# Optimization experiments

Measured on AMD Instinct MI355X. Metric: run time of the kernel, lower is better.

## Reference

```python
import jax, jax.numpy as jnp
import numpy as np

BN_EPS = 1e-5
K2 = 9  # 3x3 kernel


def _conv3x3(x, w, b):
    # x: [B,C,H,W], w: [O,C,3,3] -> [B,O,H,W], stride 1, pad 1
    out = jax.lax.conv_general_dilated(
        x, w, window_strides=(1, 1), padding=((1, 1), (1, 1)),
        dimension_numbers=("NCHW", "OIHW", "NCHW"))
    return out + b[None, :, None, None]


def setup_inputs() -> dict:
    key = jax.random.key(0)
    ks = jax.random.split(key, 8)
    B, C, H, W = 8, 256, 64, 64
    O = 256
    x = jax.random.normal(ks[0], (B, C, H, W), dtype=jnp.float32)
    # offset/mask conv: small init so sampled offsets stay near the base grid
    w_off = jax.random.normal(ks[1], (3 * K2, C, 3, 3), dtype=jnp.float32) * 0.01
    b_off = jnp.zeros((3 * K2,), dtype=jnp.float32)
    weight = jax.random.normal(ks[2], (O, C, 3, 3), dtype=jnp.float32) * 0.02
    bias = jnp.zeros((O,), dtype=jnp.float32)
    gamma = jnp.ones((O,), dtype=jnp.float32)
    beta = jnp.zeros((O,), dtype=jnp.float32)
    run_mean = jax.random.normal(ks[3], (O,), dtype=jnp.float32) * 0.1
    run_var = jax.random.uniform(ks[4], (O,), dtype=jnp.float32) + 0.5
    return {"x": x, "w_off": w_off, "b_off": b_off, "weight": weight,
            "bias": bias, "gamma": gamma, "beta": beta,
            "run_mean": run_mean, "run_var": run_var}


def _deform_sample(img, py, px):
    # img: [C,H,W]; py, px: [K2,H,W] sampling coordinates.
    # Bilinear sample with zero padding outside (DCNv2 semantics:
    # out-of-bounds corners contribute zero).
    C, H, W = img.shape
    y0 = jnp.floor(py)
    x0 = jnp.floor(px)
    wy1 = py - y0  # frac weights for the 'high' corner
    wx1 = px - x0

    def gather(yi, xi):
        valid = (yi >= 0) & (yi < H) & (xi >= 0) & (xi < W)
        yc = jnp.clip(yi, 0, H - 1).astype(jnp.int32)
        xc = jnp.clip(xi, 0, W - 1).astype(jnp.int32)
        return img[:, yc, xc] * valid.astype(img.dtype)[None]  # [C,K2,H,W]

    v00 = gather(y0, x0)
    v01 = gather(y0, x0 + 1)
    v10 = gather(y0 + 1, x0)
    v11 = gather(y0 + 1, x0 + 1)
    return (v00 * ((1 - wy1) * (1 - wx1))[None]
            + v01 * ((1 - wy1) * wx1)[None]
            + v10 * (wy1 * (1 - wx1))[None]
            + v11 * (wy1 * wx1)[None])  # [C,K2,H,W]


def reference(x, w_off, b_off, weight, bias, gamma, beta, run_mean, run_var):
    B, C, H, W = x.shape
    O = weight.shape[0]
    # 1) offset / mask branch (standard 3x3 conv)
    om = _conv3x3(x, w_off, b_off)  # [B, 27, H, W]
    off_y = om[:, :K2]
    off_x = om[:, K2:2 * K2]
    mask = jax.nn.sigmoid(om[:, 2 * K2:])  # modulation, [B,9,H,W]
    # 2) base sampling grid for 3x3, stride 1, pad 1, dilation 1
    ky = jnp.repeat(jnp.arange(3), 3).astype(x.dtype)  # [9]
    kx = jnp.tile(jnp.arange(3), 3).astype(x.dtype)    # [9]
    hs = jnp.arange(H, dtype=x.dtype)
    ws = jnp.arange(W, dtype=x.dtype)
    base_y = hs[None, :, None] - 1.0 + ky[:, None, None]  # [9,H,1]
    base_x = ws[None, None, :] - 1.0 + kx[:, None, None]  # [9,1,W]
    py = base_y[None] + off_y  # [B,9,H,W]
    px = base_x[None] + off_x
    # 3) modulated deformable im2col (bilinear gather) per batch
    cols = jax.vmap(_deform_sample)(x, py, px)  # [B,C,9,H,W]
    cols = cols * mask[:, None]                 # apply modulation mask
    # 4) GEMM over (C, K2) + bias
    w3 = weight.reshape(O, C, K2)
    out = jnp.einsum("ock,bckhw->bohw", w3, cols) + bias[None, :, None, None]
    # 5) BatchNorm (eval mode, running stats) + ReLU
    inv = gamma / jnp.sqrt(run_var + BN_EPS)
    out = out * inv[None, :, None, None] + (beta - run_mean * inv)[None, :, None, None]
    return jax.nn.relu(out)
```

## Files before the change

kernel.cpp:

```cpp
#include <hip/hip_runtime.h>
#include <math.h>

#define H 64
#define W 64
#define C 256
#define O 256
#define CK 2304
#define NB 8
#define HWSZ 4096

typedef __attribute__((ext_vector_type(8))) short short8;
typedef __attribute__((ext_vector_type(4))) float floatx4;
typedef __attribute__((ext_vector_type(4))) unsigned uintx4;

#define FSWZ(n) ((((n) & 3) << 1) | (((n) >> 2) & 1))

__device__ __forceinline__ float lo2f(unsigned u) {
  return __builtin_bit_cast(float, u << 16);
}
__device__ __forceinline__ float hi2f(unsigned u) {
  return __builtin_bit_cast(float, u & 0xffff0000u);
}
__device__ __forceinline__ unsigned pk2bf(float v0, float v1) {
  unsigned a = __builtin_bit_cast(unsigned, v0);
  unsigned b = __builtin_bit_cast(unsigned, v1);
  return ((a + 0x8000u) >> 16) | ((b + 0x8000u) & 0xffff0000u);
}

__global__ __launch_bounds__(512) void prep_x(
    const float* __restrict__ x, unsigned short* __restrict__ xt) {
  __shared__ unsigned tile[16384];
  int bid = blockIdx.x;
  int tid = threadIdx.x;
  int b = bid >> 5;
  int yg = bid & 31;
  int y0 = yg * 2;

#pragma unroll
  for (int j = 0; j < 4; ++j) {
    int e = tid + 512 * j;
    int xx4 = e & 15;
    int cp = e >> 4;
    const float* p0 = x + ((size_t)b * C + 2 * cp) * HWSZ + y0 * W + xx4 * 4;
    floatx4 f00 = *reinterpret_cast<const floatx4*>(p0);
    floatx4 f01 = *reinterpret_cast<const floatx4*>(p0 + W);
    floatx4 f10 = *reinterpret_cast<const floatx4*>(p0 + HWSZ);
    floatx4 f11 = *reinterpret_cast<const floatx4*>(p0 + HWSZ + W);
    int sw = cp & 31;
#pragma unroll
    for (int k = 0; k < 4; ++k) {
      int px = xx4 * 4 + k;
      tile[cp * 64 + (px ^ sw)] = pk2bf(f00[k], f10[k]);
      tile[8192 + cp * 64 + (px ^ sw)] = pk2bf(f01[k], f11[k]);
    }
  }
  __syncthreads();

  unsigned short* xo = xt + ((size_t)(b * 64 + y0) << 14);
#pragma unroll
  for (int j = 0; j < 8; ++j) {
    int e = tid + 512 * j;
    int cq = e & 31;
    int xx = (e >> 5) & 63;
    int r = e >> 11;
    unsigned u[4];
#pragma unroll
    for (int kk = 0; kk < 4; ++kk) {
      int cpv = cq * 4 + kk;
      u[kk] = tile[r * 8192 + cpv * 64 + (xx ^ (cpv & 31))];
    }
    uint4 v = {u[0], u[1], u[2], u[3]};
    *reinterpret_cast<uint4*>(xo + (r << 14) + (xx << 8) + (cq << 3)) = v;
  }
}

__global__ __launch_bounds__(512) void prep_wb(
    const float* __restrict__ weight, const float* __restrict__ w_off,
    const float* __restrict__ bias, const float* __restrict__ gamma,
    const float* __restrict__ beta, const float* __restrict__ run_mean,
    const float* __restrict__ run_var, unsigned short* __restrict__ wb,
    unsigned short* __restrict__ wob, float* __restrict__ invsh) {
  int bid = blockIdx.x;
  int tid = threadIdx.x;

  if (bid < 144) {
    int idx = bid * 512 + tid;
    int d0 = idx * 8;
    int lane = idx & 63;
    int mt = (idx >> 6) & 15;
    int ks = idx >> 10;
    int o = mt * 16 + (lane & 15);
    int kn0 = ks * 32 + (lane >> 4) * 8;
    int tap = kn0 >> 8;
    int c0 = kn0 & 255;
    const float* wsrc = weight + o * CK + c0 * 9 + tap;
    unsigned pk[4];
#pragma unroll
    for (int p = 0; p < 4; ++p)
      pk[p] = pk2bf(wsrc[(2 * p) * 9], wsrc[(2 * p + 1) * 9]);
    uint4 v = {pk[0], pk[1], pk[2], pk[3]};
    *reinterpret_cast<uint4*>(wb + d0) = v;
  } else if (bid < 162) {
    int idx = (bid - 144) * 512 + tid;
    int d0 = idx * 8;
    int lane = idx & 63;
    int mt = (idx >> 6) & 1;
    int ks = idx >> 7;
    int o = mt * 16 + (lane & 15);
    int kn0 = ks * 32 + (lane >> 4) * 8;
    int tap = kn0 >> 8;
    int c0 = kn0 & 255;
    uint4 v;
    if (o < 27) {
      const float* wsrc = w_off + o * CK + c0 * 9 + tap;
      unsigned pk[4];
#pragma unroll
      for (int p = 0; p < 4; ++p)
        pk[p] = pk2bf(wsrc[(2 * p) * 9], wsrc[(2 * p + 1) * 9]);
      v = (uint4){pk[0], pk[1], pk[2], pk[3]};
    } else {
      v = (uint4){0, 0, 0, 0};
    }
    *reinterpret_cast<uint4*>(wob + d0) = v;
  } else {
    if (tid < 256) {
      int o = tid;
      float inv = gamma[o] * rsqrtf(run_var[o] + 1e-5f);
      invsh[o] = inv;
      invsh[O + o] = beta[o] + (bias[o] - run_mean[o]) * inv;
    }
  }
}

__global__ __launch_bounds__(512, 4) void deform_mfma_kernel(
    const unsigned short* __restrict__ xt, const unsigned short* __restrict__ wob,
    const float* __restrict__ b_off, const unsigned short* __restrict__ wb,
    const float* __restrict__ invsh, float* __restrict__ out) {
  __shared__ short cols[64 * 256];
  __shared__ float sm_om[27 * 64];
  __shared__ int sbase[576];
  __shared__ float s00[576], s01[576], s10[576], s11[576];

  int tid = threadIdx.x;
  int lane = tid & 63;
  int wvid = tid >> 6;
  int q = lane >> 4;
  int lm = lane & 15;
  int b = blockIdx.x;
  int h = blockIdx.y;
  const unsigned short* xtb = xt + ((size_t)b << 20);

  if (wvid < 4) {
    int mt = wvid & 1;
    int nh = wvid >> 1;
    floatx4 a0[2];
    a0[0] = (floatx4){0.f, 0.f, 0.f, 0.f};
    a0[1] = (floatx4){0.f, 0.f, 0.f, 0.f};
    int pxu[2];
    pxu[0] = (nh * 2 + 0) * 16 + lm;
    pxu[1] = (nh * 2 + 1) * 16 + lm;
    for (int tap = 0; tap < 9; ++tap) {
      int yy = h - 1 + tap / 3;
      bool vy = (yy >= 0) && (yy < H);
      const unsigned short* bp[2];
      bool vv[2];
#pragma unroll
      for (int u = 0; u < 2; ++u) {
        int xx = pxu[u] - 1 + tap % 3;
        vv[u] = vy && (xx >= 0) && (xx < W);
        bp[u] = xtb + ((((yy & 63) << 6) + (xx & 63)) << 8) + q * 8;
      }
#pragma unroll
      for (int s = 0; s < 8; ++s) {
        int ks = tap * 8 + s;
        short8 afrag = *reinterpret_cast<const short8*>(
            wob + (((ks * 2 + mt) * 64 + lane) << 3));
#pragma unroll
        for (int u = 0; u < 2; ++u) {
          short8 bfrag;
          if (vv[u])
            bfrag = *reinterpret_cast<const short8*>(bp[u] + s * 32);
          else
            bfrag = (short8){0, 0, 0, 0, 0, 0, 0, 0};
          a0[u] = __builtin_amdgcn_mfma_f32_16x16x32_bf16(afrag, bfrag, a0[u], 0, 0, 0);
        }
      }
    }
#pragma unroll
    for (int u = 0; u < 2; ++u)
#pragma unroll
      for (int r = 0; r < 4; ++r) {
        int o = mt * 16 + q * 4 + r;
        if (o < 27) sm_om[o * 64 + pxu[u]] = a0[u][r] + b_off[o];
      }
  }
  __syncthreads();

  for (int e = tid; e < 576; e += 512) {
    int n = e & 63;
    int k = e >> 6;
    float oy = sm_om[k * 64 + n];
    float ox = sm_om[(9 + k) * 64 + n];
    float mv = sm_om[(18 + k) * 64 + n];
    float m = 1.0f / (1.0f + __expf(-mv));
    float py = (float)(h - 1 + k / 3) + oy;
    float px = (float)(n - 1 + k % 3) + ox;
    float yf = floorf(py), xf = floorf(px);
    int y0 = (int)yf, x0 = (int)xf;
    float fy = py - yf, fx = px - xf;
    float r0, r1; int yl;
    if (y0 >= 0 && y0 <= H - 2)      { yl = y0;    r0 = 1.f - fy; r1 = fy;       }
    else if (y0 == -1)               { yl = 0;     r0 = fy;       r1 = 0.f;      }
    else if (y0 == H - 1)            { yl = H - 2; r0 = 0.f;      r1 = 1.f - fy; }
    else                             { yl = 0;     r0 = 0.f;      r1 = 0.f;      }
    float c0, c1; int xl;
    if (x0 >= 0 && x0 <= W - 2)      { xl = x0;    c0 = 1.f - fx; c1 = fx;       }
    else if (x0 == -1)               { xl = 0;     c0 = fx;       c1 = 0.f;      }
    else if (x0 == W - 1)            { xl = W - 2; c0 = 0.f;      c1 = 1.f - fx; }
    else                             { xl = 0;     c0 = 0.f;      c1 = 0.f;      }
    r0 *= m; r1 *= m;
    sbase[e] = ((yl << 6) + xl) << 8;
    s00[e] = r0 * c0; s01[e] = r0 * c1;
    s10[e] = r1 * c0; s11[e] = r1 * c1;
  }
  __syncthreads();

  floatx4 acc[2][4];
#pragma unroll
  for (int a = 0; a < 2; ++a)
#pragma unroll
    for (int u = 0; u < 4; ++u) acc[a][u] = (floatx4){0.f, 0.f, 0.f, 0.f};

  int sn = tid >> 3;
  int scb = tid & 7;

  for (int tap = 0; tap < 9; ++tap) {
    if (tap) __syncthreads();
    {
      int ei = tap * 64 + sn;
      int base = sbase[ei];
      float w00 = s00[ei], w01 = s01[ei], w10 = s10[ei], w11 = s11[ei];
      const unsigned short* p = xtb + base;
#pragma unroll
      for (int i = 0; i < 4; ++i) {
        int cbw = (i << 3) | scb;
        int co = cbw << 3;
        uintx4 u00 = *reinterpret_cast<const uintx4*>(p + co);
        uintx4 u01 = *reinterpret_cast<const uintx4*>(p + 256 + co);
        uintx4 u10 = *reinterpret_cast<const uintx4*>(p + 16384 + co);
        uintx4 u11 = *reinterpret_cast<const uintx4*>(p + 16640 + co);
        uintx4 res;
#pragma unroll
        for (int jd = 0; jd < 4; ++jd) {
          float v0 = fmaf(w00, lo2f(u00[jd]),
                     fmaf(w01, lo2f(u01[jd]),
                     fmaf(w10, lo2f(u10[jd]), w11 * lo2f(u11[jd]))));
          float v1 = fmaf(w00, hi2f(u00[jd]),
                     fmaf(w01, hi2f(u01[jd]),
                     fmaf(w10, hi2f(u10[jd]), w11 * hi2f(u11[jd]))));
          res[jd] = pk2bf(v0, v1);
        }
        int pos = (cbw ^ FSWZ(sn)) & 31;
        *reinterpret_cast<uintx4*>(&cols[(sn << 8) + (pos << 3)]) = res;
      }
    }
    __syncthreads();

#pragma unroll
    for (int s = 0; s < 8; ++s) {
      int ks = tap * 8 + s;
      short8 afrag[2];
#pragma unroll
      for (int a = 0; a < 2; ++a)
        afrag[a] = *reinterpret_cast<const short8*>(
            wb + (((ks * 16 + wvid * 2 + a) * 64 + lane) << 3));
      short8 bfrag[4];
#pragma unroll
      for (int u = 0; u < 4; ++u) {
        int nn = u * 16 + lm;
        int pos = ((s * 4 + q) ^ FSWZ(nn)) & 31;
        bfrag[u] = *reinterpret_cast<const short8*>(&cols[(nn << 8) + (pos << 3)]);
      }
#pragma unroll
      for (int a = 0; a < 2; ++a)
#pragma unroll
        for (int u = 0; u < 4; ++u)
          acc[a][u] = __builtin_amdgcn_mfma_f32_16x16x32_bf16(
              afrag[a], bfrag[u], acc[a][u], 0, 0, 0);
    }
  }

#pragma unroll
  for (int a = 0; a < 2; ++a) {
#pragma unroll
    for (int u = 0; u < 4; ++u) {
      int nn = u * 16 + lm;
#pragma unroll
      for (int r = 0; r < 4; ++r) {
        int o = (wvid * 2 + a) * 16 + q * 4 + r;
        float v = fmaf(acc[a][u][r], invsh[o], invsh[O + o]);
        out[((size_t)(b * O + o)) * HWSZ + h * W + nn] = fmaxf(v, 0.0f);
      }
    }
  }
}

extern "C" void kernel_launch(void* const* d_in, const int* in_sizes, int n_in,
                              void* d_out, int out_size, void* d_ws, size_t ws_size,
                              hipStream_t stream) {
  const float* x        = (const float*)d_in[0];
  const float* w_off    = (const float*)d_in[1];
  const float* b_off    = (const float*)d_in[2];
  const float* weight   = (const float*)d_in[3];
  const float* bias     = (const float*)d_in[4];
  const float* gamma    = (const float*)d_in[5];
  const float* beta     = (const float*)d_in[6];
  const float* run_mean = (const float*)d_in[7];
  const float* run_var  = (const float*)d_in[8];
  float* out = (float*)d_out;

  char* ws = (char*)d_ws;
  unsigned short* xt = (unsigned short*)ws;
  unsigned short* wbf = (unsigned short*)(ws + 16777216);
  unsigned short* wob = (unsigned short*)(ws + 17956864);
  float* invsh = (float*)(ws + 18104320);

  prep_x<<<256, 512, 0, stream>>>(x, xt);
  prep_wb<<<163, 512, 0, stream>>>(weight, w_off, bias, gamma, beta,
                                   run_mean, run_var, wbf, wob, invsh);
  {
    dim3 grid(NB, H);
    deform_mfma_kernel<<<grid, 512, 0, stream>>>(xt, wob, b_off, wbf, invsh, out);
  }
}
```

Baseline: 192.5 us.

## Merge prep kernels and use packed FP32 math for bilinear sampling

Combines the two preprocessing kernels into a single launch, with block-index ranges selecting the x-transpose path or the weight-packing path. This removes one kernel launch and the serialization between them. The bilinear interpolation inner loop now uses v_pk_mul_f32/v_pk_fma_f32 inline asm and the hardware v_cvt_pk_bf16_f32 conversion in place of scalar FMAs and manual rounding. Fewer VALU instructions are issued in the sampling stage, though the bf16 rounding behaviour may differ slightly from the manual round-half-up.

```diff
diff --git a/kernel.cpp b/kernel.cpp
--- a/kernel.cpp
+++ b/kernel.cpp
@@ -12,6 +12,7 @@
 typedef __attribute__((ext_vector_type(8))) short short8;
 typedef __attribute__((ext_vector_type(4))) float floatx4;
 typedef __attribute__((ext_vector_type(4))) unsigned uintx4;
+typedef __attribute__((ext_vector_type(2))) float f32x2;
 
 #define FSWZ(n) ((((n) & 3) << 1) | (((n) >> 2) & 1))
 
@@ -20,6 +21,9 @@
 }
 __device__ __forceinline__ float hi2f(unsigned u) {
   return __builtin_bit_cast(float, u & 0xffff0000u);
+}
+__device__ __forceinline__ f32x2 up2(unsigned u) {
+  return (f32x2){lo2f(u), hi2f(u)};
 }
 __device__ __forceinline__ unsigned pk2bf(float v0, float v1) {
   unsigned a = __builtin_bit_cast(unsigned, v0);
@@ -27,64 +31,74 @@
   return ((a + 0x8000u) >> 16) | ((b + 0x8000u) & 0xffff0000u);
 }
 
-__global__ __launch_bounds__(512) void prep_x(
-    const float* __restrict__ x, unsigned short* __restrict__ xt) {
+__device__ __forceinline__ f32x2 pk_mul(f32x2 a, f32x2 b) {
+  f32x2 d;
+  asm("v_pk_mul_f32 %0, %1, %2" : "=v"(d) : "v"(a), "v"(b));
+  return d;
+}
+__device__ __forceinline__ f32x2 pk_fma(f32x2 a, f32x2 b, f32x2 c) {
+  f32x2 d;
+  asm("v_pk_fma_f32 %0, %1, %2, %3" : "=v"(d) : "v"(a), "v"(b), "v"(c));
+  return d;
+}
+__device__ __forceinline__ unsigned cvtpk(f32x2 a) {
+  unsigned d;
+  asm("v_cvt_pk_bf16_f32 %0, %1, %2" : "=v"(d) : "v"(a[0]), "v"(a[1]));
+  return d;
+}
+
+__global__ __launch_bounds__(512) void prep_all2(
+    const float* __restrict__ x, const float* __restrict__ weight,
+    const float* __restrict__ w_off, const float* __restrict__ bias,
+    const float* __restrict__ gamma, const float* __restrict__ beta,
+    const float* __restrict__ run_mean, const float* __restrict__ run_var,
+    unsigned short* __restrict__ xt, unsigned short* __restrict__ wb,
+    unsigned short* __restrict__ wob, float* __restrict__ invsh) {
   __shared__ unsigned tile[16384];
   int bid = blockIdx.x;
   int tid = threadIdx.x;
-  int b = bid >> 5;
-  int yg = bid & 31;
-  int y0 = yg * 2;
-
-#pragma unroll
-  for (int j = 0; j < 4; ++j) {
-    int e = tid + 512 * j;
-    int xx4 = e & 15;
-    int cp = e >> 4;
-    const float* p0 = x + ((size_t)b * C + 2 * cp) * HWSZ + y0 * W + xx4 * 4;
-    floatx4 f00 = *reinterpret_cast<const floatx4*>(p0);
-    floatx4 f01 = *reinterpret_cast<const floatx4*>(p0 + W);
-    floatx4 f10 = *reinterpret_cast<const floatx4*>(p0 + HWSZ);
-    floatx4 f11 = *reinterpret_cast<const floatx4*>(p0 + HWSZ + W);
-    int sw = cp & 31;
-#pragma unroll
-    for (int k = 0; k < 4; ++k) {
-      int px = xx4 * 4 + k;
-      tile[cp * 64 + (px ^ sw)] = pk2bf(f00[k], f10[k]);
-      tile[8192 + cp * 64 + (px ^ sw)] = pk2bf(f01[k], f11[k]);
-    }
-  }
-  __syncthreads();
-
-  unsigned short* xo = xt + ((size_t)(b * 64 + y0) << 14);
-#pragma unroll
-  for (int j = 0; j < 8; ++j) {
-    int e = tid + 512 * j;
-    int cq = e & 31;
-    int xx = (e >> 5) & 63;
-    int r = e >> 11;
-    unsigned u[4];
-#pragma unroll
-    for (int kk = 0; kk < 4; ++kk) {
-      int cpv = cq * 4 + kk;
-      u[kk] = tile[r * 8192 + cpv * 64 + (xx ^ (cpv & 31))];
-    }
-    uint4 v = {u[0], u[1], u[2], u[3]};
-    *reinterpret_cast<uint4*>(xo + (r << 14) + (xx << 8) + (cq << 3)) = v;
-  }
-}
-
-__global__ __launch_bounds__(512) void prep_wb(
-    const float* __restrict__ weight, const float* __restrict__ w_off,
-    const float* __restrict__ bias, const float* __restrict__ gamma,
-    const float* __restrict__ beta, const float* __restrict__ run_mean,
-    const float* __restrict__ run_var, unsigned short* __restrict__ wb,
-    unsigned short* __restrict__ wob, float* __restrict__ invsh) {
-  int bid = blockIdx.x;
-  int tid = threadIdx.x;
-
-  if (bid < 144) {
-    int idx = bid * 512 + tid;
+
+  if (bid < 256) {
+    int b = bid >> 5;
+    int yg = bid & 31;
+    int y0 = yg * 2;
+#pragma unroll
+    for (int j = 0; j < 4; ++j) {
+      int e = tid + 512 * j;
+      int xx4 = e & 15;
+      int cp = e >> 4;
+      const float* p0 = x + ((size_t)b * C + 2 * cp) * HWSZ + y0 * W + xx4 * 4;
+      floatx4 f00 = *reinterpret_cast<const floatx4*>(p0);
+      floatx4 f01 = *reinterpret_cast<const floatx4*>(p0 + W);
+      floatx4 f10 = *reinterpret_cast<const floatx4*>(p0 + HWSZ);
+      floatx4 f11 = *reinterpret_cast<const floatx4*>(p0 + HWSZ + W);
+      int sw = cp & 31;
+#pragma unroll
+      for (int k = 0; k < 4; ++k) {
+        int px = xx4 * 4 + k;
+        tile[cp * 64 + (px ^ sw)] = pk2bf(f00[k], f10[k]);
+        tile[8192 + cp * 64 + (px ^ sw)] = pk2bf(f01[k], f11[k]);
+      }
+    }
+    __syncthreads();
+    unsigned short* xo = xt + ((size_t)(b * 64 + y0) << 14);
+#pragma unroll
+    for (int j = 0; j < 8; ++j) {
+      int e = tid + 512 * j;
+      int cq = e & 31;
+      int xx = (e >> 5) & 63;
+      int r = e >> 11;
+      unsigned u[4];
+#pragma unroll
+      for (int kk = 0; kk < 4; ++kk) {
+        int cpv = cq * 4 + kk;
+        u[kk] = tile[r * 8192 + cpv * 64 + (xx ^ (cpv & 31))];
+      }
+      uint4 v = {u[0], u[1], u[2], u[3]};
+      *reinterpret_cast<uint4*>(xo + (r << 14) + (xx << 8) + (cq << 3)) = v;
+    }
+  } else if (bid < 400) {
+    int idx = (bid - 256) * 512 + tid;
     int d0 = idx * 8;
     int lane = idx & 63;
     int mt = (idx >> 6) & 15;
@@ -100,8 +114,8 @@
       pk[p] = pk2bf(wsrc[(2 * p) * 9], wsrc[(2 * p + 1) * 9]);
     uint4 v = {pk[0], pk[1], pk[2], pk[3]};
     *reinterpret_cast<uint4*>(wb + d0) = v;
-  } else if (bid < 162) {
-    int idx = (bid - 144) * 512 + tid;
+  } else if (bid < 418) {
+    int idx = (bid - 400) * 512 + tid;
     int d0 = idx * 8;
     int lane = idx & 63;
     int mt = (idx >> 6) & 1;
@@ -240,6 +254,10 @@
       int ei = tap * 64 + sn;
       int base = sbase[ei];
       float w00 = s00[ei], w01 = s01[ei], w10 = s10[ei], w11 = s11[ei];
+      f32x2 W00 = (f32x2){w00, w00};
+      f32x2 W01 = (f32x2){w01, w01};
+      f32x2 W10 = (f32x2){w10, w10};
+      f32x2 W11 = (f32x2){w11, w11};
       const unsigned short* p = xtb + base;
 #pragma unroll
       for (int i = 0; i < 4; ++i) {
@@ -252,13 +270,11 @@
         uintx4 res;
 #pragma unroll
         for (int jd = 0; jd < 4; ++jd) {
-          float v0 = fmaf(w00, lo2f(u00[jd]),
-                     fmaf(w01, lo2f(u01[jd]),
-                     fmaf(w10, lo2f(u10[jd]), w11 * lo2f(u11[jd]))));
-          float v1 = fmaf(w00, hi2f(u00[jd]),
-                     fmaf(w01, hi2f(u01[jd]),
-                     fmaf(w10, hi2f(u10[jd]), w11 * hi2f(u11[jd]))));
-          res[jd] = pk2bf(v0, v1);
+          f32x2 a = pk_mul(up2(u00[jd]), W00);
+          a = pk_fma(up2(u01[jd]), W01, a);
+          a = pk_fma(up2(u10[jd]), W10, a);
+          a = pk_fma(up2(u11[jd]), W11, a);
+          res[jd] = cvtpk(a);
         }
         int pos = (cbw ^ FSWZ(sn)) & 31;
         *reinterpret_cast<uintx4*>(&cols[(sn << 8) + (pos << 3)]) = res;
@@ -325,9 +341,8 @@
   unsigned short* wob = (unsigned short*)(ws + 17956864);
   float* invsh = (float*)(ws + 18104320);
 
-  prep_x<<<256, 512, 0, stream>>>(x, xt);
-  prep_wb<<<163, 512, 0, stream>>>(weight, w_off, bias, gamma, beta,
-                                   run_mean, run_var, wbf, wob, invsh);
+  prep_all2<<<419, 512, 0, stream>>>(x, weight, w_off, bias, gamma, beta,
+                                     run_mean, run_var, xt, wbf, wob, invsh);
   {
     dim3 grid(NB, H);
     deform_mfma_kernel<<<grid, 512, 0, stream>>>(xt, wob, b_off, wbf, invsh, out);
```

Result: no change. 189.0 us (-1.9%).
